# Performance work log

Hardware: AMD Instinct MI355X
Metric: run time of the kernel (lower is better)

The kernel has to match this reference:

```python
import jax, jax.numpy as jnp
import numpy as np

B = 64
T0_V = 512   # existing timesteps already in the graph memory
TAU_V = 128  # new timesteps inserted this call
NTOT = T0_V + TAU_V  # 640 == graph_size
FEAT = 256
K = 16       # causal temporal window (edges j->i for j in [i-K, i))


def _build_edges():
    # per-batch causal edges, then offset by b*NTOT into the flat graph
    src_l, dst_l = [], []
    for off in range(1, K + 1):
        ii = np.arange(off, NTOT)
        src_l.append(ii - off)
        dst_l.append(ii)
    src = np.concatenate(src_l)
    dst = np.concatenate(dst_l)
    boff = (np.arange(B) * NTOT)[:, None]
    edge_src = (src[None, :] + boff).reshape(-1)
    edge_dst = (dst[None, :] + boff).reshape(-1)
    return jnp.asarray(edge_src, jnp.int32), jnp.asarray(edge_dst, jnp.int32)


def setup_inputs() -> dict:
    key = jax.random.key(0)
    ks = jax.random.split(key, 8)
    x = jax.random.normal(ks[0], (B, TAU_V, FEAT), jnp.float32)
    nodes = 0.1 * jax.random.normal(ks[1], (B, NTOT, FEAT), jnp.float32)
    edge_src, edge_dst = _build_edges()
    E = edge_src.shape[0]
    edge_weight = jnp.ones((E,), jnp.float32)
    sc = 1.0 / np.sqrt(FEAT)
    W1_self = sc * jax.random.normal(ks[2], (FEAT, FEAT), jnp.float32)
    W1_nbr = sc * jax.random.normal(ks[3], (FEAT, FEAT), jnp.float32)
    b1 = jnp.zeros((FEAT,), jnp.float32)
    W2_self = sc * jax.random.normal(ks[4], (FEAT, FEAT), jnp.float32)
    W2_nbr = sc * jax.random.normal(ks[5], (FEAT, FEAT), jnp.float32)
    b2 = jnp.zeros((FEAT,), jnp.float32)
    return {"x": x, "nodes": nodes, "edge_weight": edge_weight,
            "W1_self": W1_self, "W1_nbr": W1_nbr, "b1": b1,
            "W2_self": W2_self, "W2_nbr": W2_nbr, "b2": b2,
            "edge_src": edge_src, "edge_dst": edge_dst,
            "T0": T0_V, "tau": TAU_V}


def reference(x, nodes, edge_weight, W1_self, W1_nbr, b1, W2_self, W2_nbr, b2,
              edge_src, edge_dst, T0, tau):
    Bv, t, feat = x.shape
    ntot = T0 + tau
    # scatter new observations into the node memory (uniform taus -> dense slice)
    nodes = nodes.at[:, T0:T0 + tau, :].set(x)
    # adj normalization: values / values.detach() == 1 in the forward pass
    w = edge_weight / jax.lax.stop_gradient(edge_weight)
    # flatten per-batch ragged graphs (regular here since taus are uniform)
    flat = nodes[:, :ntot].reshape(Bv * ntot, feat)  # [B*ntot, feat]
    nseg = Bv * ntot

    def gconv(h, Ws, Wn, b):
        msg = h[edge_src] * w[:, None]                       # [E, d] gather
        agg = jax.ops.segment_sum(msg, edge_dst, num_segments=nseg)
        return jnp.tanh(h @ Ws + agg @ Wn + b)

    h = gconv(flat, W1_self, W1_nbr, b1)
    h = gconv(h, W2_self, W2_nbr, b2)
    # gather outputs for the newly-inserted nodes -> [B, tau, out_feat]
    out_idx = (jnp.arange(Bv)[:, None] * ntot + T0 + jnp.arange(tau)[None, :]).reshape(-1)
    mx_dense = h[out_idx].reshape(Bv, tau, -1)
    return mx_dense
```

## Files before the change

kernel.cpp:

```cpp
#include <hip/hip_runtime.h>
#include <hip/hip_bf16.h>


namespace {

constexpr int BQ    = 64;
constexpr int FEATC = 256;
constexpr int M1 = 144;
constexpr int M2 = 128;

using ushort = unsigned short;
using short8 = __attribute__((ext_vector_type(8))) short;
using f32x4  = __attribute__((ext_vector_type(4))) float;

__device__ __forceinline__ ushort f2bf(float f) {
  union { float f; unsigned u; } v{f};
  unsigned r = v.u + 0x7FFFu + ((v.u >> 16) & 1u);
  return (ushort)(r >> 16);
}
__device__ __forceinline__ float bf2f(ushort h) {
  union { unsigned u; float f; } v{(unsigned)h << 16};
  return v.f;
}
__device__ __forceinline__ void split2(float v, ushort& hi, ushort& lo) {
  hi = f2bf(v);
  lo = f2bf(v - bf2f(hi));
}
__device__ __forceinline__ float tanh_fast(float x) {
  const float e = __builtin_amdgcn_exp2f(x * 2.8853900817779268f);
  return 1.0f - 2.0f * __builtin_amdgcn_rcpf(1.0f + e);
}
__device__ __forceinline__ void gl_lds16(const ushort* g, ushort* l) {
  __builtin_amdgcn_global_load_lds(
      (const __attribute__((address_space(1))) void*)g,
      (__attribute__((address_space(3))) void*)l, 16, 0, 0);
}

__device__ __forceinline__ size_t frag_idx(int row, int k, int s) {
  return ((size_t)(((row >> 4) * 16 + (k >> 5)) * 2 + s)) * 512
       + ((k >> 3) & 3) * 128 + (row & 15) * 8 + (k & 7);
}
__device__ __forceinline__ int lofs(int row_l, int k, int s) {
  return ((k >> 5) * 2 + s) * 512 + ((k >> 3) & 3) * 128 + row_l * 8 + (k & 7);
}

__global__ __launch_bounds__(256) void prep_fused(
    const float* __restrict__ x, const float* __restrict__ nodes,
    const float* __restrict__ W1s, const float* __restrict__ W1n,
    const float* __restrict__ W2s, const float* __restrict__ W2n,
    ushort* __restrict__ A1F, ushort* __restrict__ WF1,
    ushort* __restrict__ WF2) {
  __shared__ ushort lds_o[16384];
  __shared__ float tile[64][65];
  const int blk = blockIdx.x;
  if (blk < 576) {
    const int G = 4 * (blk % 144) + (blk / 144);
    const int b = G / 9, c = G % 9, f = threadIdx.x;
    const int t0 = c * 16, i0 = 496 + t0;
    const float* nb = nodes + ((size_t)b * 640) * FEATC + f;
    const float* xb = x     + ((size_t)b * 128) * FEATC + f;

    float v[32];
    #pragma unroll
    for (int d = 0; d < 32; ++d) {
      const int i = i0 - 16 + d;
      v[d] = (i < 512) ? nb[(size_t)i * FEATC] : xb[(size_t)(i - 512) * FEATC];
    }
    float win = 0.f;
    #pragma unroll
    for (int d = 0; d < 16; ++d) win += v[d];

    #pragma unroll
    for (int tt = 0; tt < 16; ++tt) {
      ushort hi, lo;
      split2(v[16 + tt], hi, lo);
      lds_o[lofs(tt, f, 0)] = hi;
      lds_o[lofs(tt, f, 1)] = lo;
      split2(win, hi, lo);
      lds_o[lofs(tt, 256 + f, 0)] = hi;
      lds_o[lofs(tt, 256 + f, 1)] = lo;
      win += v[16 + tt] - v[tt];
    }
    __syncthreads();
    ushort* dst = A1F + (size_t)G * 16384;
    #pragma unroll
    for (int it = 0; it < 8; ++it) {
      const int idx = it * 256 + threadIdx.x;
      *(short8*)(dst + idx * 8) = *(const short8*)(lds_o + idx * 8);
    }
  } else {
    const int w = blk - 576;
    const int z = w >> 4, rem = w & 15;
    const int k0 = (rem >> 2) * 64, n0 = (rem & 3) * 64;
    const float* src = (z == 0) ? W1s : (z == 1) ? W1n : (z == 2) ? W2s : W2n;
    ushort* dst = (z < 2) ? WF1 : WF2;
    const int koff = (z & 1) * 256;
    const int c = threadIdx.x & 63, r4 = threadIdx.x >> 6;
    #pragma unroll
    for (int p = 0; p < 16; ++p) {
      const int k = r4 + p * 4;
      tile[k][c] = src[(size_t)(k0 + k) * FEATC + n0 + c];
    }
    __syncthreads();
    #pragma unroll
    for (int p = 0; p < 16; ++p) {
      const int n = r4 + p * 4;
      ushort hi, lo;
      split2(tile[c][n], hi, lo);
      dst[frag_idx(n0 + n, koff + k0 + c, 0)] = hi;
      dst[frag_idx(n0 + n, koff + k0 + c, 1)] = lo;
    }
  }
}

#define GLOAD(dst, ptr)                                                      \
  asm volatile("global_load_dwordx4 %0, %1, off"                             \
               : "=v"(dst) : "v"(ptr) : "memory")

#define WAITV(n) do {                                                        \
  asm volatile("s_waitcnt vmcnt(" #n ")" ::: "memory");                      \
  __builtin_amdgcn_sched_barrier(0);                                         \
} while (0)

#define MF(a, b, c) c = __builtin_amdgcn_mfma_f32_16x16x32_bf16(a, b, c, 0, 0, 0)

#define STAGEA(jn, kb) do {                                                  \
  gl_lds16(srcu0 + (kb) * 1024, sbase + (jn) * 5120 + u0 * 512);             \
  gl_lds16(srcu1 + (kb) * 1024, sbase + (jn) * 5120 + u1 * 512);             \
  if (g3) gl_lds16(srcu2 + (kb) * 1024, sbase + (jn) * 5120 + u2 * 512);     \
} while (0)

#define WAITW1 do { if (g3) { WAITV(5); } else { WAITV(4); } } while (0)

#define COMPJ2(j, WH, WL) do {                                               \
  const ushort* bp_ = sbase + (j) * 5120 + lane * 8;                         \
  const short8 a0h = *(const short8*)(bp_ + 0 * 512);                        \
  const short8 a0l = *(const short8*)(bp_ + 1 * 512);                        \
  const short8 a1h = *(const short8*)(bp_ + 2 * 512);                        \
  const short8 a1l = *(const short8*)(bp_ + 3 * 512);                        \
  const short8 a2h = *(const short8*)(bp_ + 4 * 512);                        \
  const short8 a2l = *(const short8*)(bp_ + 5 * 512);                        \
  const short8 a3h = *(const short8*)(bp_ + 6 * 512);                        \
  const short8 a3l = *(const short8*)(bp_ + 7 * 512);                        \
  const short8 a4h = *(const short8*)(bp_ + 8 * 512);                        \
  const short8 a4l = *(const short8*)(bp_ + 9 * 512);                        \
  __builtin_amdgcn_s_setprio(1);                                            \
  MF(a0h, WH, acc[0]); MF(a1h, WH, acc[1]); MF(a2h, WH, acc[2]);             \
  MF(a3h, WH, acc[3]); MF(a4h, WH, acc[4]);                                  \
  MF(a0h, WL, acc[0]); MF(a1h, WL, acc[1]); MF(a2h, WL, acc[2]);             \
  MF(a3h, WL, acc[3]); MF(a4h, WL, acc[4]);                                  \
  MF(a0l, WH, acc[0]); MF(a1l, WH, acc[1]); MF(a2l, WH, acc[2]);             \
  MF(a3l, WH, acc[3]); MF(a4l, WH, acc[4]);                                  \
  __builtin_amdgcn_s_setprio(0);                                            \
  __builtin_amdgcn_sched_barrier(0);                                        \
} while (0)

#define HALF1(j, ks, js, WH, WL, NWH, NWL) do {                              \
  COMPJ2(j, WH, WL);                                                         \
  STAGEA(js, ks);                                                            \
  GLOAD(NWH, bW + (ks) * 1024); GLOAD(NWL, bW + (ks) * 1024 + 512);          \
} while (0)

__global__ __launch_bounds__(256, 2) void gemm1_fused(
    const ushort* __restrict__ A, const ushort* __restrict__ W,
    const float* __restrict__ bias, ushort* __restrict__ A2F) {
  __shared__ __align__(16) unsigned char ldsmem[54528];
  ushort* sbase = (ushort*)ldsmem;
  float (*hvt)[68] = (float(*)[68])ldsmem;
  ushort* outb = (ushort*)(ldsmem + 21760);

  const int tid = threadIdx.x;
  const int wave = tid >> 6, lane = tid & 63;
  const int lr = lane & 15, kg = lane >> 4;
  const int mx2 = blockIdx.x, ny = blockIdx.y;
  const int b = mx2 >> 1, half = mx2 & 1;
  const int rgA0 = 9 * b + 4 * half;
  const int n0 = ny * 64;
  const int ngw = ny * 4 + wave;

  const bool g3 = (wave < 2);
  const int uw = g3 ? wave * 3 : 6 + (wave - 2) * 2;
  const int u0 = uw, u1 = uw + 1, u2 = g3 ? uw + 2 : uw + 1;
  auto srcA = [&](int u) {
    return A + ((size_t)(rgA0 + (u >> 1)) * 32 + (u & 1)) * 512 + lane * 8;
  };
  const ushort* srcu0 = srcA(u0);
  const ushort* srcu1 = srcA(u1);
  const ushort* srcu2 = srcA(u2);

  const ushort* bW = W + (size_t)ngw * 16384 + lane * 8;

  f32x4 acc[5] = {};
  short8 w0h, w0l, w1h, w1l, w2h, w2l, w3h, w3l, w4h, w4l;

  STAGEA(0, 0); GLOAD(w0h, bW);        GLOAD(w0l, bW + 512);
  STAGEA(1, 1); GLOAD(w1h, bW + 1024); GLOAD(w1l, bW + 1536);
  STAGEA(2, 2); GLOAD(w2h, bW + 2048); GLOAD(w2l, bW + 2560);

  WAITW1; __builtin_amdgcn_s_barrier();
  HALF1(0, 3, 3, w0h, w0l, w3h, w3l);  HALF1(1, 4, 4, w1h, w1l, w4h, w4l);
  WAITW1; __builtin_amdgcn_s_barrier();
  HALF1(2, 5, 0, w2h, w2l, w0h, w0l);  HALF1(3, 6, 1, w3h, w3l, w1h, w1l);
  WAITW1; __builtin_amdgcn_s_barrier();
  HALF1(4, 7, 2, w4h, w4l, w2h, w2l);  HALF1(0, 8, 3, w0h, w0l, w3h, w3l);
  WAITW1; __builtin_amdgcn_s_barrier();
  HALF1(1, 9, 4, w1h, w1l, w4h, w4l);  HALF1(2, 10, 0, w2h, w2l, w0h, w0l);
  WAITW1; __builtin_amdgcn_s_barrier();
  HALF1(3, 11, 1, w3h, w3l, w1h, w1l); HALF1(4, 12, 2, w4h, w4l, w2h, w2l);
  WAITW1; __builtin_amdgcn_s_barrier();
  HALF1(0, 13, 3, w0h, w0l, w3h, w3l); HALF1(1, 14, 4, w1h, w1l, w4h, w4l);
  WAITW1; __builtin_amdgcn_s_barrier();
  HALF1(2, 15, 0, w2h, w2l, w0h, w0l); COMPJ2(3, w3h, w3l);
  WAITV(0); __builtin_amdgcn_s_barrier();
  COMPJ2(4, w4h, w4l); COMPJ2(0, w0h, w0l);

  __syncthreads();

  const float bv = bias[n0 + wave * 16 + lr];
  #pragma unroll
  for (int fr = 0; fr < 5; ++fr)
    #pragma unroll
    for (int r = 0; r < 4; ++r)
      hvt[fr * 16 + kg * 4 + r][wave * 16 + lr] = tanh_fast(acc[fr][r] + bv);
  __syncthreads();

  {
    const int col = tid & 63, q = tid >> 6;
    float hv[32];
    #pragma unroll
    for (int d = 0; d < 32; ++d) hv[d] = hvt[q * 16 + d][col];
    float win = 0.f;
    #pragma unroll
    for (int d = 0; d < 16; ++d) win += hv[d];

    const int su = ((q * 4 + (col >> 5)) * 2) * 512
                 + ((col >> 3) & 3) * 128 + (col & 7);
    const int wu = ((q * 4 + 2 + (col >> 5)) * 2) * 512
                 + ((col >> 3) & 3) * 128 + (col & 7);
    #pragma unroll
    for (int tt = 0; tt < 16; ++tt) {
      ushort hi, lo;
      split2(hv[16 + tt], hi, lo);
      outb[su + tt * 8]       = hi;
      outb[su + tt * 8 + 512] = lo;
      split2(win, hi, lo);
      outb[wu + tt * 8]       = hi;
      outb[wu + tt * 8 + 512] = lo;
      win += hv[16 + tt] - hv[tt];
    }
  }
  __syncthreads();

  const int rg20 = 4 * mx2;
  #pragma unroll
  for (int it = 0; it < 8; ++it) {
    const int lin = it * 2048 + tid * 8;
    const int u = lin >> 9, w = lin & 511;
    const int uq = u >> 3, ukbl = (u >> 1) & 3, us = u & 1;
    const int KB = (ukbl < 2) ? (2 * ny + ukbl) : (8 + 2 * ny + (ukbl - 2));
    const size_t dst = ((size_t)((rg20 + uq) * 16 + KB) * 2 + us) * 512 + w;
    *(short8*)(A2F + dst) = *(const short8*)(outb + lin);
  }
}

#define STAGE2(jn, kb) do {                                                  \
  gl_lds16(srcv0 + (kb) * 1024, sb2 + (jn) * 4096 + v0 * 512);               \
  gl_lds16(srcv1 + (kb) * 1024, sb2 + (jn) * 4096 + v1 * 512);               \
} while (0)

#define COMPK(j, WH, WL) do {                                                \
  const ushort* bp_ = sb2 + (j) * 4096 + lane * 8;                           \
  const short8 a0h = *(const short8*)(bp_ + 0 * 512);                        \
  const short8 a0l = *(const short8*)(bp_ + 1 * 512);                        \
  const short8 a1h = *(const short8*)(bp_ + 2 * 512);                        \
  const short8 a1l = *(const short8*)(bp_ + 3 * 512);                        \
  const short8 a2h = *(const short8*)(bp_ + 4 * 512);                        \
  const short8 a2l = *(const short8*)(bp_ + 5 * 512);                        \
  const short8 a3h = *(const short8*)(bp_ + 6 * 512);                        \
  const short8 a3l = *(const short8*)(bp_ + 7 * 512);                        \
  __builtin_amdgcn_s_setprio(1);                                            \
  MF(a0h, WH, acc[0]); MF(a1h, WH, acc[1]);                                  \
  MF(a2h, WH, acc[2]); MF(a3h, WH, acc[3]);                                  \
  MF(a0h, WL, acc[0]); MF(a1h, WL, acc[1]);                                  \
  MF(a2h, WL, acc[2]); MF(a3h, WL, acc[3]);                                  \
  MF(a0l, WH, acc[0]); MF(a1l, WH, acc[1]);                                  \
  MF(a2l, WH, acc[2]); MF(a3l, WH, acc[3]);                                  \
  __builtin_amdgcn_s_setprio(0);                                            \
  __builtin_amdgcn_sched_barrier(0);                                        \
} while (0)

#define HALF2(j, ks, js, WH, WL, NWH, NWL) do {                              \
  COMPK(j, WH, WL);                                                          \
  STAGE2(js, ks);                                                            \
  GLOAD(NWH, bW + (ks) * 1024); GLOAD(NWL, bW + (ks) * 1024 + 512);          \
} while (0)

__global__ __launch_bounds__(256, 2) void gemm2_lds(
    const ushort* __restrict__ A, const ushort* __restrict__ W,
    const float* __restrict__ bias, float* __restrict__ out) {
  __shared__ __align__(16) unsigned char lds2[40960];
  ushort* sb2 = (ushort*)lds2;
  float (*tile)[68] = (float(*)[68])lds2;

  const int tid = threadIdx.x;
  const int wave = tid >> 6, lane = tid & 63;
  const int lr = lane & 15, kg = lane >> 4;
  const int mx = blockIdx.x, ny2 = blockIdx.y;
  const int rg0 = mx * 4;
  const int ngw = ny2 * 4 + wave;
  const int n0col = ngw * 16;

  const int v0 = wave * 2, v1 = wave * 2 + 1;
  auto srcA = [&](int u) {
    return A + ((size_t)(rg0 + (u >> 1)) * 32 + (u & 1)) * 512 + lane * 8;
  };
  const ushort* srcv0 = srcA(v0);
  const ushort* srcv1 = srcA(v1);
  const ushort* bW = W + (size_t)ngw * 16384 + lane * 8;

  f32x4 acc[4] = {};
  short8 w0h, w0l, w1h, w1l, w2h, w2l, w3h, w3l, w4h, w4l;

  STAGE2(0, 0); GLOAD(w0h, bW);        GLOAD(w0l, bW + 512);
  STAGE2(1, 1); GLOAD(w1h, bW + 1024); GLOAD(w1l, bW + 1536);
  STAGE2(2, 2); GLOAD(w2h, bW + 2048); GLOAD(w2l, bW + 2560);

  WAITV(4); __builtin_amdgcn_s_barrier();
  HALF2(0, 3, 3, w0h, w0l, w3h, w3l);  HALF2(1, 4, 4, w1h, w1l, w4h, w4l);
  WAITV(4); __builtin_amdgcn_s_barrier();
  HALF2(2, 5, 0, w2h, w2l, w0h, w0l);  HALF2(3, 6, 1, w3h, w3l, w1h, w1l);
  WAITV(4); __builtin_amdgcn_s_barrier();
  HALF2(4, 7, 2, w4h, w4l, w2h, w2l);  HALF2(0, 8, 3, w0h, w0l, w3h, w3l);
  WAITV(4); __builtin_amdgcn_s_barrier();
  HALF2(1, 9, 4, w1h, w1l, w4h, w4l);  HALF2(2, 10, 0, w2h, w2l, w0h, w0l);
  WAITV(4); __builtin_amdgcn_s_barrier();
  HALF2(3, 11, 1, w3h, w3l, w1h, w1l); HALF2(4, 12, 2, w4h, w4l, w2h, w2l);
  WAITV(4); __builtin_amdgcn_s_barrier();
  HALF2(0, 13, 3, w0h, w0l, w3h, w3l); HALF2(1, 14, 4, w1h, w1l, w4h, w4l);
  WAITV(4); __builtin_amdgcn_s_barrier();
  HALF2(2, 15, 0, w2h, w2l, w0h, w0l); COMPK(3, w3h, w3l);
  WAITV(0); __builtin_amdgcn_s_barrier();
  COMPK(4, w4h, w4l); COMPK(0, w0h, w0l);

  __syncthreads();
  const float bv = bias[n0col + lr];
  #pragma unroll
  for (int fr = 0; fr < 4; ++fr)
    #pragma unroll
    for (int r = 0; r < 4; ++r)
      tile[fr * 16 + kg * 4 + r][wave * 16 + lr] = tanh_fast(acc[fr][r] + bv);
  __syncthreads();
  #pragma unroll
  for (int it = 0; it < 4; ++it) {
    const int idx = it * 256 + tid;
    const int row = idx >> 4, ch = idx & 15;
    *(f32x4*)(out + (size_t)(mx * 64 + row) * FEATC + ny2 * 64 + ch * 4) =
        *(const f32x4*)&tile[row][ch * 4];
  }
}

}

extern "C" void kernel_launch(void* const* d_in, const int* in_sizes, int n_in,
                              void* d_out, int out_size, void* d_ws, size_t ws_size,
                              hipStream_t stream) {
  const float* x     = (const float*)d_in[0];
  const float* nodes = (const float*)d_in[1];
  const float* W1s = (const float*)d_in[3];
  const float* W1n = (const float*)d_in[4];
  const float* b1  = (const float*)d_in[5];
  const float* W2s = (const float*)d_in[6];
  const float* W2n = (const float*)d_in[7];
  const float* b2  = (const float*)d_in[8];
  float* out = (float*)d_out;

  const size_t a1_sz = (size_t)BQ * M1 * 1024;
  const size_t a2_sz = (size_t)BQ * M2 * 1024;
  const size_t wf_sz = (size_t)16 * 16 * 2 * 512;
  const size_t need = (a1_sz + a2_sz + 2 * wf_sz) * sizeof(ushort);
  if (ws_size < need) return;

  ushort* p = (ushort*)d_ws;
  ushort* A1F = p; p += a1_sz;
  ushort* A2F = p; p += a2_sz;
  ushort* WF1 = p; p += wf_sz;
  ushort* WF2 = p; p += wf_sz;

  prep_fused<<<640, 256, 0, stream>>>(x, nodes, W1s, W1n, W2s, W2n,
                                      A1F, WF1, WF2);
  gemm1_fused<<<dim3(BQ * 2, FEATC / 64), 256, 0, stream>>>(A1F, WF1, b1, A2F);
  gemm2_lds<<<dim3((BQ * M2) / 64, FEATC / 64), 256, 0, stream>>>(
      A2F, WF2, b2, out);
}
```

Measured before the change: 36.06 us.

## Apply neighbor weight before window sum to halve GEMM K dimension

Uses linearity: instead of building a windowed-sum aggregate as extra K columns (K=512) and multiplying by concatenated weights, both GEMMs now compute Q = h·Wn and P = h·Ws on the raw rows (K=256). The 16-step sliding-window sum is then applied to Q in the epilogue before bias and tanh. This roughly halves the prep output and the GEMM K loop, and drops the windowed-sum tiles from the layer-1 intermediate, at the cost of more epilogue work and redundant halo rows. Work is regrouped per batch, and gemm1 occupancy rises to 3 blocks.

```diff
diff --git a/kernel.cpp b/kernel.cpp
--- a/kernel.cpp
+++ b/kernel.cpp
@@ -6,8 +6,6 @@
 
 constexpr int BQ    = 64;
 constexpr int FEATC = 256;
-constexpr int M1 = 144;
-constexpr int M2 = 128;
 
 using ushort = unsigned short;
 using short8 = __attribute__((ext_vector_type(8))) short;
@@ -36,66 +34,52 @@
       (__attribute__((address_space(3))) void*)l, 16, 0, 0);
 }
 
-__device__ __forceinline__ size_t frag_idx(int row, int k, int s) {
-  return ((size_t)(((row >> 4) * 16 + (k >> 5)) * 2 + s)) * 512
-       + ((k >> 3) & 3) * 128 + (row & 15) * 8 + (k & 7);
-}
 __device__ __forceinline__ int lofs(int row_l, int k, int s) {
   return ((k >> 5) * 2 + s) * 512 + ((k >> 3) & 3) * 128 + row_l * 8 + (k & 7);
 }
-
-__global__ __launch_bounds__(256) void prep_fused(
+__device__ __forceinline__ size_t wfrag(int n, int k, int s) {
+  return ((size_t)(((n >> 4) * 8 + (k >> 5)) * 2 + s)) * 512
+       + ((k >> 3) & 3) * 128 + (n & 15) * 8 + (k & 7);
+}
+
+__global__ __launch_bounds__(256) void prep_all(
     const float* __restrict__ x, const float* __restrict__ nodes,
     const float* __restrict__ W1s, const float* __restrict__ W1n,
     const float* __restrict__ W2s, const float* __restrict__ W2n,
-    ushort* __restrict__ A1F, ushort* __restrict__ WF1,
-    ushort* __restrict__ WF2) {
-  __shared__ ushort lds_o[16384];
+    ushort* __restrict__ NF, ushort* __restrict__ WS1,
+    ushort* __restrict__ WN1, ushort* __restrict__ WS2,
+    ushort* __restrict__ WN2) {
+  __shared__ __align__(16) ushort lds_o[8192];
   __shared__ float tile[64][65];
-  const int blk = blockIdx.x;
-  if (blk < 576) {
-    const int G = 4 * (blk % 144) + (blk / 144);
-    const int b = G / 9, c = G % 9, f = threadIdx.x;
-    const int t0 = c * 16, i0 = 496 + t0;
+  const int blk = blockIdx.x, tid = threadIdx.x;
+  if (blk < 640) {
+    const int b = blk / 10, rg = blk % 10, f = tid;
     const float* nb = nodes + ((size_t)b * 640) * FEATC + f;
     const float* xb = x     + ((size_t)b * 128) * FEATC + f;
-
-    float v[32];
-    #pragma unroll
-    for (int d = 0; d < 32; ++d) {
-      const int i = i0 - 16 + d;
-      v[d] = (i < 512) ? nb[(size_t)i * FEATC] : xb[(size_t)(i - 512) * FEATC];
-    }
-    float win = 0.f;
-    #pragma unroll
-    for (int d = 0; d < 16; ++d) win += v[d];
-
     #pragma unroll
     for (int tt = 0; tt < 16; ++tt) {
+      const int i = 480 + rg * 16 + tt;
+      const float v = (i < 512) ? nb[(size_t)i * FEATC]
+                                : xb[(size_t)(i - 512) * FEATC];
       ushort hi, lo;
-      split2(v[16 + tt], hi, lo);
+      split2(v, hi, lo);
       lds_o[lofs(tt, f, 0)] = hi;
       lds_o[lofs(tt, f, 1)] = lo;
-      split2(win, hi, lo);
-      lds_o[lofs(tt, 256 + f, 0)] = hi;
-      lds_o[lofs(tt, 256 + f, 1)] = lo;
-      win += v[16 + tt] - v[tt];
     }
     __syncthreads();
-    ushort* dst = A1F + (size_t)G * 16384;
-    #pragma unroll
-    for (int it = 0; it < 8; ++it) {
-      const int idx = it * 256 + threadIdx.x;
+    ushort* dst = NF + (size_t)(b * 10 + rg) * 8192;
+    #pragma unroll
+    for (int it = 0; it < 4; ++it) {
+      const int idx = it * 256 + tid;
       *(short8*)(dst + idx * 8) = *(const short8*)(lds_o + idx * 8);
     }
   } else {
-    const int w = blk - 576;
+    const int w = blk - 640;
     const int z = w >> 4, rem = w & 15;
     const int k0 = (rem >> 2) * 64, n0 = (rem & 3) * 64;
     const float* src = (z == 0) ? W1s : (z == 1) ? W1n : (z == 2) ? W2s : W2n;
-    ushort* dst = (z < 2) ? WF1 : WF2;
-    const int koff = (z & 1) * 256;
-    const int c = threadIdx.x & 63, r4 = threadIdx.x >> 6;
+    ushort* dst = (z == 0) ? WS1 : (z == 1) ? WN1 : (z == 2) ? WS2 : WN2;
+    const int c = tid & 63, r4 = tid >> 6;
     #pragma unroll
     for (int p = 0; p < 16; ++p) {
       const int k = r4 + p * 4;
@@ -107,8 +91,8 @@
       const int n = r4 + p * 4;
       ushort hi, lo;
       split2(tile[c][n], hi, lo);
-      dst[frag_idx(n0 + n, koff + k0 + c, 0)] = hi;
-      dst[frag_idx(n0 + n, koff + k0 + c, 1)] = lo;
+      dst[wfrag(n0 + n, k0 + c, 0)] = hi;
+      dst[wfrag(n0 + n, k0 + c, 1)] = lo;
     }
   }
 }
@@ -124,16 +108,144 @@
 
 #define MF(a, b, c) c = __builtin_amdgcn_mfma_f32_16x16x32_bf16(a, b, c, 0, 0, 0)
 
-#define STAGEA(jn, kb) do {                                                  \
-  gl_lds16(srcu0 + (kb) * 1024, sbase + (jn) * 5120 + u0 * 512);             \
-  gl_lds16(srcu1 + (kb) * 1024, sbase + (jn) * 5120 + u1 * 512);             \
-  if (g3) gl_lds16(srcu2 + (kb) * 1024, sbase + (jn) * 5120 + u2 * 512);     \
-} while (0)
-
-#define WAITW1 do { if (g3) { WAITV(5); } else { WAITV(4); } } while (0)
-
-#define COMPJ2(j, WH, WL) do {                                               \
-  const ushort* bp_ = sbase + (j) * 5120 + lane * 8;                         \
+struct W4 { short8 sh, sl, nh, nl; };
+#define LW(S, bWS, bWN, kb) do {                                             \
+  GLOAD(S.sh, bWS + (kb) * 1024); GLOAD(S.sl, bWS + (kb) * 1024 + 512);      \
+  GLOAD(S.nh, bWN + (kb) * 1024); GLOAD(S.nl, bWN + (kb) * 1024 + 512);      \
+} while (0)
+
+#define STG1(jn, kb) do {                                                    \
+  gl_lds16(srcA0 + (kb) * 1024, sb1 + (jn) * 4096 + u0 * 512);               \
+  gl_lds16(srcA1 + (kb) * 1024, sb1 + (jn) * 4096 + u1 * 512);               \
+} while (0)
+
+#define COMP1(j, Wt) do {                                                    \
+  const ushort* bp_ = sb1 + (j) * 4096 + lane * 8;                           \
+  const short8 a0h = *(const short8*)(bp_ + 0 * 512);                        \
+  const short8 a0l = *(const short8*)(bp_ + 1 * 512);                        \
+  const short8 a1h = *(const short8*)(bp_ + 2 * 512);                        \
+  const short8 a1l = *(const short8*)(bp_ + 3 * 512);                        \
+  const short8 a2h = *(const short8*)(bp_ + 4 * 512);                        \
+  const short8 a2l = *(const short8*)(bp_ + 5 * 512);                        \
+  const short8 a3h = *(const short8*)(bp_ + 6 * 512);                        \
+  const short8 a3l = *(const short8*)(bp_ + 7 * 512);                        \
+  __builtin_amdgcn_s_setprio(1);                                            \
+  MF(a0h, Wt.nh, Q[0]); MF(a1h, Wt.nh, Q[1]);                                \
+  MF(a2h, Wt.nh, Q[2]); MF(a3h, Wt.nh, Q[3]);                                \
+  MF(a0h, Wt.nl, Q[0]); MF(a1h, Wt.nl, Q[1]);                                \
+  MF(a2h, Wt.nl, Q[2]); MF(a3h, Wt.nl, Q[3]);                                \
+  MF(a0l, Wt.nh, Q[0]); MF(a1l, Wt.nh, Q[1]);                                \
+  MF(a2l, Wt.nh, Q[2]); MF(a3l, Wt.nh, Q[3]);                                \
+  MF(a1h, Wt.sh, P[0]); MF(a2h, Wt.sh, P[1]); MF(a3h, Wt.sh, P[2]);          \
+  MF(a1h, Wt.sl, P[0]); MF(a2h, Wt.sl, P[1]); MF(a3h, Wt.sl, P[2]);          \
+  MF(a1l, Wt.sh, P[0]); MF(a2l, Wt.sh, P[1]); MF(a3l, Wt.sh, P[2]);          \
+  __builtin_amdgcn_s_setprio(0);                                            \
+  __builtin_amdgcn_sched_barrier(0);                                        \
+} while (0)
+
+__global__ __launch_bounds__(256, 3) void gemm1_lin(
+    const ushort* __restrict__ NF, const ushort* __restrict__ WS,
+    const ushort* __restrict__ WN, const float* __restrict__ bias,
+    ushort* __restrict__ H1F) {
+  __shared__ __align__(16) unsigned char ldsmem[42752];
+  ushort* sb1 = (ushort*)ldsmem;
+  float (*Qt)[68] = (float(*)[68])ldsmem;
+  float (*Pt)[68] = (float(*)[68])(ldsmem + 17408);
+  ushort* outb = (ushort*)(ldsmem + 30464);
+
+  const int tid = threadIdx.x;
+  const int wave = tid >> 6, lane = tid & 63;
+  const int lr = lane & 15, kg = lane >> 4;
+  const int mx = blockIdx.x, ny = blockIdx.y;
+  const int b = mx / 3, sub = mx % 3;
+  const int rgN0 = 3 * sub;
+  const int ngw = ny * 4 + wave;
+
+  const int u0 = wave * 2, u1 = wave * 2 + 1;
+  const ushort* srcA0 =
+      NF + ((size_t)((b * 10 + rgN0 + (u0 >> 1)) * 16) + (u0 & 1)) * 512 + lane * 8;
+  const ushort* srcA1 =
+      NF + ((size_t)((b * 10 + rgN0 + (u1 >> 1)) * 16) + (u1 & 1)) * 512 + lane * 8;
+  const ushort* bWS = WS + (size_t)ngw * 8192 + lane * 8;
+  const ushort* bWN = WN + (size_t)ngw * 8192 + lane * 8;
+
+  f32x4 Q[4] = {}, P[3] = {};
+  W4 w0, w1, w2;
+
+  STG1(0, 0); LW(w0, bWS, bWN, 0);
+  STG1(1, 1); LW(w1, bWS, bWN, 1);
+
+  WAITV(6); __builtin_amdgcn_s_barrier(); COMP1(0, w0);
+  STG1(2, 2); LW(w2, bWS, bWN, 2);
+  WAITV(6); __builtin_amdgcn_s_barrier(); COMP1(1, w1);
+  STG1(0, 3); LW(w0, bWS, bWN, 3);
+  WAITV(6); __builtin_amdgcn_s_barrier(); COMP1(2, w2);
+  STG1(1, 4); LW(w1, bWS, bWN, 4);
+  WAITV(6); __builtin_amdgcn_s_barrier(); COMP1(0, w0);
+  STG1(2, 5); LW(w2, bWS, bWN, 5);
+  WAITV(6); __builtin_amdgcn_s_barrier(); COMP1(1, w1);
+  STG1(0, 6); LW(w0, bWS, bWN, 6);
+  WAITV(6); __builtin_amdgcn_s_barrier(); COMP1(2, w2);
+  STG1(1, 7); LW(w1, bWS, bWN, 7);
+  WAITV(6); __builtin_amdgcn_s_barrier(); COMP1(0, w0);
+  WAITV(0); __builtin_amdgcn_s_barrier(); COMP1(1, w1);
+
+  __syncthreads();
+
+  #pragma unroll
+  for (int fr = 0; fr < 4; ++fr)
+    #pragma unroll
+    for (int r = 0; r < 4; ++r)
+      Qt[fr * 16 + kg * 4 + r][wave * 16 + lr] = Q[fr][r];
+  #pragma unroll
+  for (int p = 0; p < 3; ++p)
+    #pragma unroll
+    for (int r = 0; r < 4; ++r)
+      Pt[p * 16 + kg * 4 + r][wave * 16 + lr] = P[p][r];
+  __syncthreads();
+
+  {
+    const int col = tid & 63, q = tid >> 6;
+    const float bv = bias[ny * 64 + col];
+    const int t0 = q * 12;
+    float win = 0.f;
+    #pragma unroll
+    for (int d = 0; d < 16; ++d) win += Qt[t0 + d][col];
+    for (int tt = 0; tt < 12; ++tt) {
+      const int t = t0 + tt;
+      const float h = tanh_fast(Pt[t][col] + win + bv);
+      ushort hi, lo;
+      split2(h, hi, lo);
+      const int base = (((t >> 4) * 2 + (col >> 5)) * 2) * 512
+                     + ((col >> 3) & 3) * 128 + (t & 15) * 8 + (col & 7);
+      outb[base]       = hi;
+      outb[base + 512] = lo;
+      if (tt < 11) win += Qt[t + 16][col] - Qt[t][col];
+    }
+  }
+  __syncthreads();
+
+  #pragma unroll
+  for (int it = 0; it < 3; ++it) {
+    const int lin = it * 2048 + tid * 8;
+    const int u = lin >> 9, w = lin & 511;
+    const int lrg = u >> 2, lkb = (u >> 1) & 1, s = u & 1;
+    const size_t dst =
+        ((size_t)((b * 9 + 3 * sub + lrg) * 8 + ny * 2 + lkb) * 2 + s) * 512 + w;
+    *(short8*)(H1F + dst) = *(const short8*)(outb + lin);
+  }
+}
+
+#define STG2(jn, kb) do {                                                    \
+  gl_lds16(srcB0 + (kb) * 1024, sb2 + (jn) * 5120 + v0 * 512);               \
+  gl_lds16(srcB1 + (kb) * 1024, sb2 + (jn) * 5120 + v1 * 512);               \
+  if (g3) gl_lds16(srcB2 + (kb) * 1024, sb2 + (jn) * 5120 + v2 * 512);       \
+} while (0)
+
+#define WAITW do { if (g3) { WAITV(7); } else { WAITV(6); } } while (0)
+
+#define COMP2(j, Wt) do {                                                    \
+  const ushort* bp_ = sb2 + (j) * 5120 + lane * 8;                           \
   const short8 a0h = *(const short8*)(bp_ + 0 * 512);                        \
   const short8 a0l = *(const short8*)(bp_ + 1 * 512);                        \
   const short8 a1h = *(const short8*)(bp_ + 2 * 512);                        \
@@ -145,217 +257,109 @@
   const short8 a4h = *(const short8*)(bp_ + 8 * 512);                        \
   const short8 a4l = *(const short8*)(bp_ + 9 * 512);                        \
   __builtin_amdgcn_s_setprio(1);                                            \
-  MF(a0h, WH, acc[0]); MF(a1h, WH, acc[1]); MF(a2h, WH, acc[2]);             \
-  MF(a3h, WH, acc[3]); MF(a4h, WH, acc[4]);                                  \
-  MF(a0h, WL, acc[0]); MF(a1h, WL, acc[1]); MF(a2h, WL, acc[2]);             \
-  MF(a3h, WL, acc[3]); MF(a4h, WL, acc[4]);                                  \
-  MF(a0l, WH, acc[0]); MF(a1l, WH, acc[1]); MF(a2l, WH, acc[2]);             \
-  MF(a3l, WH, acc[3]); MF(a4l, WH, acc[4]);                                  \
+  MF(a0h, Wt.nh, Q[0]); MF(a1h, Wt.nh, Q[1]); MF(a2h, Wt.nh, Q[2]);          \
+  MF(a3h, Wt.nh, Q[3]); MF(a4h, Wt.nh, Q[4]);                                \
+  MF(a0h, Wt.nl, Q[0]); MF(a1h, Wt.nl, Q[1]); MF(a2h, Wt.nl, Q[2]);          \
+  MF(a3h, Wt.nl, Q[3]); MF(a4h, Wt.nl, Q[4]);                                \
+  MF(a0l, Wt.nh, Q[0]); MF(a1l, Wt.nh, Q[1]); MF(a2l, Wt.nh, Q[2]);          \
+  MF(a3l, Wt.nh, Q[3]); MF(a4l, Wt.nh, Q[4]);                                \
+  MF(a1h, Wt.sh, P[0]); MF(a2h, Wt.sh, P[1]);                                \
+  MF(a3h, Wt.sh, P[2]); MF(a4h, Wt.sh, P[3]);                                \
+  MF(a1h, Wt.sl, P[0]); MF(a2h, Wt.sl, P[1]);                                \
+  MF(a3h, Wt.sl, P[2]); MF(a4h, Wt.sl, P[3]);                                \
+  MF(a1l, Wt.sh, P[0]); MF(a2l, Wt.sh, P[1]);                                \
+  MF(a3l, Wt.sh, P[2]); MF(a4l, Wt.sh, P[3]);                                \
   __builtin_amdgcn_s_setprio(0);                                            \
   __builtin_amdgcn_sched_barrier(0);                                        \
 } while (0)
 
-#define HALF1(j, ks, js, WH, WL, NWH, NWL) do {                              \
-  COMPJ2(j, WH, WL);                                                         \
-  STAGEA(js, ks);                                                            \
-  GLOAD(NWH, bW + (ks) * 1024); GLOAD(NWL, bW + (ks) * 1024 + 512);          \
-} while (0)
-
-__global__ __launch_bounds__(256, 2) void gemm1_fused(
-    const ushort* __restrict__ A, const ushort* __restrict__ W,
-    const float* __restrict__ bias, ushort* __restrict__ A2F) {
-  __shared__ __align__(16) unsigned char ldsmem[54528];
-  ushort* sbase = (ushort*)ldsmem;
-  float (*hvt)[68] = (float(*)[68])ldsmem;
-  ushort* outb = (ushort*)(ldsmem + 21760);
+__global__ __launch_bounds__(256, 2) void gemm2_lin(
+    const ushort* __restrict__ H1F, const ushort* __restrict__ WS,
+    const ushort* __restrict__ WN, const float* __restrict__ bias,
+    float* __restrict__ out) {
+  __shared__ __align__(16) unsigned char ldsmem[39168];
+  ushort* sb2 = (ushort*)ldsmem;
+  float (*Qt)[68] = (float(*)[68])ldsmem;
+  float (*Pt)[68] = (float(*)[68])(ldsmem + 21760);
 
   const int tid = threadIdx.x;
   const int wave = tid >> 6, lane = tid & 63;
   const int lr = lane & 15, kg = lane >> 4;
-  const int mx2 = blockIdx.x, ny = blockIdx.y;
-  const int b = mx2 >> 1, half = mx2 & 1;
-  const int rgA0 = 9 * b + 4 * half;
-  const int n0 = ny * 64;
+  const int mx = blockIdx.x, ny = blockIdx.y;
+  const int b = mx >> 1, h = mx & 1;
+  const int rgH0 = 4 * h;
   const int ngw = ny * 4 + wave;
 
   const bool g3 = (wave < 2);
-  const int uw = g3 ? wave * 3 : 6 + (wave - 2) * 2;
-  const int u0 = uw, u1 = uw + 1, u2 = g3 ? uw + 2 : uw + 1;
-  auto srcA = [&](int u) {
-    return A + ((size_t)(rgA0 + (u >> 1)) * 32 + (u & 1)) * 512 + lane * 8;
+  const int vw = g3 ? wave * 3 : 6 + (wave - 2) * 2;
+  const int v0 = vw, v1 = vw + 1, v2 = g3 ? vw + 2 : vw + 1;
+  auto srcH = [&](int u) {
+    return H1F + ((size_t)((b * 9 + rgH0 + (u >> 1)) * 16) + (u & 1)) * 512
+           + lane * 8;
   };
-  const ushort* srcu0 = srcA(u0);
-  const ushort* srcu1 = srcA(u1);
-  const ushort* srcu2 = srcA(u2);
-
-  const ushort* bW = W + (size_t)ngw * 16384 + lane * 8;
-
-  f32x4 acc[5] = {};
-  short8 w0h, w0l, w1h, w1l, w2h, w2l, w3h, w3l, w4h, w4l;
-
-  STAGEA(0, 0); GLOAD(w0h, bW);        GLOAD(w0l, bW + 512);
-  STAGEA(1, 1); GLOAD(w1h, bW + 1024); GLOAD(w1l, bW + 1536);
-  STAGEA(2, 2); GLOAD(w2h, bW + 2048); GLOAD(w2l, bW + 2560);
-
-  WAITW1; __builtin_amdgcn_s_barrier();
-  HALF1(0, 3, 3, w0h, w0l, w3h, w3l);  HALF1(1, 4, 4, w1h, w1l, w4h, w4l);
-  WAITW1; __builtin_amdgcn_s_barrier();
-  HALF1(2, 5, 0, w2h, w2l, w0h, w0l);  HALF1(3, 6, 1, w3h, w3l, w1h, w1l);
-  WAITW1; __builtin_amdgcn_s_barrier();
-  HALF1(4, 7, 2, w4h, w4l, w2h, w2l);  HALF1(0, 8, 3, w0h, w0l, w3h, w3l);
-  WAITW1; __builtin_amdgcn_s_barrier();
-  HALF1(1, 9, 4, w1h, w1l, w4h, w4l);  HALF1(2, 10, 0, w2h, w2l, w0h, w0l);
-  WAITW1; __builtin_amdgcn_s_barrier();
-  HALF1(3, 11, 1, w3h, w3l, w1h, w1l); HALF1(4, 12, 2, w4h, w4l, w2h, w2l);
-  WAITW1; __builtin_amdgcn_s_barrier();
-  HALF1(0, 13, 3, w0h, w0l, w3h, w3l); HALF1(1, 14, 4, w1h, w1l, w4h, w4l);
-  WAITW1; __builtin_amdgcn_s_barrier();
-  HALF1(2, 15, 0, w2h, w2l, w0h, w0l); COMPJ2(3, w3h, w3l);
-  WAITV(0); __builtin_amdgcn_s_barrier();
-  COMPJ2(4, w4h, w4l); COMPJ2(0, w0h, w0l);
-
-  __syncthreads();
-
-  const float bv = bias[n0 + wave * 16 + lr];
+  const ushort* srcB0 = srcH(v0);
+  const ushort* srcB1 = srcH(v1);
+  const ushort* srcB2 = srcH(v2);
+  const ushort* bWS = WS + (size_t)ngw * 8192 + lane * 8;
+  const ushort* bWN = WN + (size_t)ngw * 8192 + lane * 8;
+
+  f32x4 Q[5] = {}, P[4] = {};
+  W4 w0, w1, w2;
+
+  STG2(0, 0); LW(w0, bWS, bWN, 0);
+  STG2(1, 1); LW(w1, bWS, bWN, 1);
+
+  WAITW; __builtin_amdgcn_s_barrier(); COMP2(0, w0);
+  STG2(2, 2); LW(w2, bWS, bWN, 2);
+  WAITW; __builtin_amdgcn_s_barrier(); COMP2(1, w1);
+  STG2(0, 3); LW(w0, bWS, bWN, 3);
+  WAITW; __builtin_amdgcn_s_barrier(); COMP2(2, w2);
+  STG2(1, 4); LW(w1, bWS, bWN, 4);
+  WAITW; __builtin_amdgcn_s_barrier(); COMP2(0, w0);
+  STG2(2, 5); LW(w2, bWS, bWN, 5);
+  WAITW; __builtin_amdgcn_s_barrier(); COMP2(1, w1);
+  STG2(0, 6); LW(w0, bWS, bWN, 6);
+  WAITW; __builtin_amdgcn_s_barrier(); COMP2(2, w2);
+  STG2(1, 7); LW(w1, bWS, bWN, 7);
+  WAITW; __builtin_amdgcn_s_barrier(); COMP2(0, w0);
+  WAITV(0); __builtin_amdgcn_s_barrier(); COMP2(1, w1);
+
+  __syncthreads();
+
   #pragma unroll
   for (int fr = 0; fr < 5; ++fr)
     #pragma unroll
     for (int r = 0; r < 4; ++r)
-      hvt[fr * 16 + kg * 4 + r][wave * 16 + lr] = tanh_fast(acc[fr][r] + bv);
+      Qt[fr * 16 + kg * 4 + r][wave * 16 + lr] = Q[fr][r];
+  #pragma unroll
+  for (int p = 0; p < 4; ++p)
+    #pragma unroll
+    for (int r = 0; r < 4; ++r)
+      Pt[p * 16 + kg * 4 + r][wave * 16 + lr] = P[p][r];
   __syncthreads();
 
   {
     const int col = tid & 63, q = tid >> 6;
-    float hv[32];
-    #pragma unroll
-    for (int d = 0; d < 32; ++d) hv[d] = hvt[q * 16 + d][col];
+    const float bv = bias[ny * 64 + col];
+    const int t0 = q * 16;
     float win = 0.f;
     #pragma unroll
-    for (int d = 0; d < 16; ++d) win += hv[d];
-
-    const int su = ((q * 4 + (col >> 5)) * 2) * 512
-                 + ((col >> 3) & 3) * 128 + (col & 7);
-    const int wu = ((q * 4 + 2 + (col >> 5)) * 2) * 512
-                 + ((col >> 3) & 3) * 128 + (col & 7);
-    #pragma unroll
+    for (int d = 0; d < 16; ++d) win += Qt[t0 + d][col];
     for (int tt = 0; tt < 16; ++tt) {
-      ushort hi, lo;
-      split2(hv[16 + tt], hi, lo);
-      outb[su + tt * 8]       = hi;
-      outb[su + tt * 8 + 512] = lo;
-      split2(win, hi, lo);
-      outb[wu + tt * 8]       = hi;
-      outb[wu + tt * 8 + 512] = lo;
-      win += hv[16 + tt] - hv[tt];
-    }
-  }
-  __syncthreads();
-
-  const int rg20 = 4 * mx2;
-  #pragma unroll
-  for (int it = 0; it < 8; ++it) {
-    const int lin = it * 2048 + tid * 8;
-    const int u = lin >> 9, w = lin & 511;
-    const int uq = u >> 3, ukbl = (u >> 1) & 3, us = u & 1;
-    const int KB = (ukbl < 2) ? (2 * ny + ukbl) : (8 + 2 * ny + (ukbl - 2));
-    const size_t dst = ((size_t)((rg20 + uq) * 16 + KB) * 2 + us) * 512 + w;
-    *(short8*)(A2F + dst) = *(const short8*)(outb + lin);
-  }
-}
-
-#define STAGE2(jn, kb) do {                                                  \
-  gl_lds16(srcv0 + (kb) * 1024, sb2 + (jn) * 4096 + v0 * 512);               \
-  gl_lds16(srcv1 + (kb) * 1024, sb2 + (jn) * 4096 + v1 * 512);               \
-} while (0)
-
-#define COMPK(j, WH, WL) do {                                                \
-  const ushort* bp_ = sb2 + (j) * 4096 + lane * 8;                           \
-  const short8 a0h = *(const short8*)(bp_ + 0 * 512);                        \
-  const short8 a0l = *(const short8*)(bp_ + 1 * 512);                        \
-  const short8 a1h = *(const short8*)(bp_ + 2 * 512);                        \
-  const short8 a1l = *(const short8*)(bp_ + 3 * 512);                        \
-  const short8 a2h = *(const short8*)(bp_ + 4 * 512);                        \
-  const short8 a2l = *(const short8*)(bp_ + 5 * 512);                        \
-  const short8 a3h = *(const short8*)(bp_ + 6 * 512);                        \
-  const short8 a3l = *(const short8*)(bp_ + 7 * 512);                        \
-  __builtin_amdgcn_s_setprio(1);                                            \
-  MF(a0h, WH, acc[0]); MF(a1h, WH, acc[1]);                                  \
-  MF(a2h, WH, acc[2]); MF(a3h, WH, acc[3]);                                  \
-  MF(a0h, WL, acc[0]); MF(a1h, WL, acc[1]);                                  \
-  MF(a2h, WL, acc[2]); MF(a3h, WL, acc[3]);                                  \
-  MF(a0l, WH, acc[0]); MF(a1l, WH, acc[1]);                                  \
-  MF(a2l, WH, acc[2]); MF(a3l, WH, acc[3]);                                  \
-  __builtin_amdgcn_s_setprio(0);                                            \
-  __builtin_amdgcn_sched_barrier(0);                                        \
-} while (0)
-
-#define HALF2(j, ks, js, WH, WL, NWH, NWL) do {                              \
-  COMPK(j, WH, WL);                                                          \
-  STAGE2(js, ks);                                                            \
-  GLOAD(NWH, bW + (ks) * 1024); GLOAD(NWL, bW + (ks) * 1024 + 512);          \
-} while (0)
-
-__global__ __launch_bounds__(256, 2) void gemm2_lds(
-    const ushort* __restrict__ A, const ushort* __restrict__ W,
-    const float* __restrict__ bias, float* __restrict__ out) {
-  __shared__ __align__(16) unsigned char lds2[40960];
-  ushort* sb2 = (ushort*)lds2;
-  float (*tile)[68] = (float(*)[68])lds2;
-
-  const int tid = threadIdx.x;
-  const int wave = tid >> 6, lane = tid & 63;
-  const int lr = lane & 15, kg = lane >> 4;
-  const int mx = blockIdx.x, ny2 = blockIdx.y;
-  const int rg0 = mx * 4;
-  const int ngw = ny2 * 4 + wave;
-  const int n0col = ngw * 16;
-
-  const int v0 = wave * 2, v1 = wave * 2 + 1;
-  auto srcA = [&](int u) {
-    return A + ((size_t)(rg0 + (u >> 1)) * 32 + (u & 1)) * 512 + lane * 8;
-  };
-  const ushort* srcv0 = srcA(v0);
-  const ushort* srcv1 = srcA(v1);
-  const ushort* bW = W + (size_t)ngw * 16384 + lane * 8;
-
-  f32x4 acc[4] = {};
-  short8 w0h, w0l, w1h, w1l, w2h, w2l, w3h, w3l, w4h, w4l;
-
-  STAGE2(0, 0); GLOAD(w0h, bW);        GLOAD(w0l, bW + 512);
-  STAGE2(1, 1); GLOAD(w1h, bW + 1024); GLOAD(w1l, bW + 1536);
-  STAGE2(2, 2); GLOAD(w2h, bW + 2048); GLOAD(w2l, bW + 2560);
-
-  WAITV(4); __builtin_amdgcn_s_barrier();
-  HALF2(0, 3, 3, w0h, w0l, w3h, w3l);  HALF2(1, 4, 4, w1h, w1l, w4h, w4l);
-  WAITV(4); __builtin_amdgcn_s_barrier();
-  HALF2(2, 5, 0, w2h, w2l, w0h, w0l);  HALF2(3, 6, 1, w3h, w3l, w1h, w1l);
-  WAITV(4); __builtin_amdgcn_s_barrier();
-  HALF2(4, 7, 2, w4h, w4l, w2h, w2l);  HALF2(0, 8, 3, w0h, w0l, w3h, w3l);
-  WAITV(4); __builtin_amdgcn_s_barrier();
-  HALF2(1, 9, 4, w1h, w1l, w4h, w4l);  HALF2(2, 10, 0, w2h, w2l, w0h, w0l);
-  WAITV(4); __builtin_amdgcn_s_barrier();
-  HALF2(3, 11, 1, w3h, w3l, w1h, w1l); HALF2(4, 12, 2, w4h, w4l, w2h, w2l);
-  WAITV(4); __builtin_amdgcn_s_barrier();
-  HALF2(0, 13, 3, w0h, w0l, w3h, w3l); HALF2(1, 14, 4, w1h, w1l, w4h, w4l);
-  WAITV(4); __builtin_amdgcn_s_barrier();
-  HALF2(2, 15, 0, w2h, w2l, w0h, w0l); COMPK(3, w3h, w3l);
-  WAITV(0); __builtin_amdgcn_s_barrier();
-  COMPK(4, w4h, w4l); COMPK(0, w0h, w0l);
-
-  __syncthreads();
-  const float bv = bias[n0col + lr];
-  #pragma unroll
-  for (int fr = 0; fr < 4; ++fr)
-    #pragma unroll
-    for (int r = 0; r < 4; ++r)
-      tile[fr * 16 + kg * 4 + r][wave * 16 + lr] = tanh_fast(acc[fr][r] + bv);
-  __syncthreads();
+      const int t = t0 + tt;
+      const float o = tanh_fast(Pt[t][col] + win + bv);
+      if (tt < 15) win += Qt[t + 16][col] - Qt[t][col];
+      Pt[t][col] = o;
+    }
+  }
+  __syncthreads();
+
   #pragma unroll
   for (int it = 0; it < 4; ++it) {
     const int idx = it * 256 + tid;
-    const int row = idx >> 4, ch = idx & 15;
-    *(f32x4*)(out + (size_t)(mx * 64 + row) * FEATC + ny2 * 64 + ch * 4) =
-        *(const f32x4*)&tile[row][ch * 4];
+    const int trow = idx >> 4, ch = idx & 15;
+    *(f32x4*)(out + (size_t)(b * 128 + 64 * h + trow) * FEATC + ny * 64 + ch * 4) =
+        *(const f32x4*)&Pt[trow][ch * 4];
   }
 }
 
@@ -374,21 +378,22 @@
   const float* b2  = (const float*)d_in[8];
   float* out = (float*)d_out;
 
-  const size_t a1_sz = (size_t)BQ * M1 * 1024;
-  const size_t a2_sz = (size_t)BQ * M2 * 1024;
-  const size_t wf_sz = (size_t)16 * 16 * 2 * 512;
-  const size_t need = (a1_sz + a2_sz + 2 * wf_sz) * sizeof(ushort);
+  const size_t nf_sz = (size_t)BQ * 10 * 8192;
+  const size_t h1_sz = (size_t)BQ * 9 * 8192;
+  const size_t w_sz  = (size_t)16 * 8 * 2 * 512;
+  const size_t need = (nf_sz + h1_sz + 4 * w_sz) * sizeof(ushort);
   if (ws_size < need) return;
 
   ushort* p = (ushort*)d_ws;
-  ushort* A1F = p; p += a1_sz;
-  ushort* A2F = p; p += a2_sz;
-  ushort* WF1 = p; p += wf_sz;
-  ushort* WF2 = p; p += wf_sz;
-
-  prep_fused<<<640, 256, 0, stream>>>(x, nodes, W1s, W1n, W2s, W2n,
-                                      A1F, WF1, WF2);
-  gemm1_fused<<<dim3(BQ * 2, FEATC / 64), 256, 0, stream>>>(A1F, WF1, b1, A2F);
-  gemm2_lds<<<dim3((BQ * M2) / 64, FEATC / 64), 256, 0, stream>>>(
-      A2F, WF2, b2, out);
-}
+  ushort* NF  = p; p += nf_sz;
+  ushort* H1F = p; p += h1_sz;
+  ushort* WS1 = p; p += w_sz;
+  ushort* WN1 = p; p += w_sz;
+  ushort* WS2 = p; p += w_sz;
+  ushort* WN2 = p; p += w_sz;
+
+  prep_all<<<704, 256, 0, stream>>>(x, nodes, W1s, W1n, W2s, W2n,
+                                    NF, WS1, WN1, WS2, WN2);
+  gemm1_lin<<<dim3(192, 4), 256, 0, stream>>>(NF, WS1, WN1, b1, H1F);
+  gemm2_lin<<<dim3(128, 4), 256, 0, stream>>>(H1F, WS2, WN2, b2, out);
+}
```

After: 37.20 us. +3.2%, slower.
